# Performance work log

Measured on AMD Instinct MI355X. Metric: run time of the kernel, lower is better.

The kernel has to match this reference:

```python
import jax, jax.numpy as jnp
import numpy as np

N, E, D, MH, C, L = 50000, 800000, 256, 256, 47, 3
BN_EPS = 1e-5
NORM_EPS = 1e-12


def setup_inputs() -> dict:
    key = jax.random.key(0)
    ks = jax.random.split(key, 20)
    s = 0.05
    inp = {
        "x": jax.random.normal(ks[0], (N, D), jnp.float32),
        "edge_index": jax.random.randint(ks[1], (2, E), 0, N, jnp.int64),
        "lin_l_W": jax.random.normal(ks[2], (L, D, D), jnp.float32) * s,
        "lin_l_b": jnp.zeros((L, D), jnp.float32),
        "lin_r_W": jax.random.normal(ks[3], (L, D, D), jnp.float32) * s,
        "lin_r_b": jnp.zeros((L, D), jnp.float32),
        "mlp_W1": jax.random.normal(ks[4], (L, D, MH), jnp.float32) * s,
        "mlp_b1": jnp.zeros((L, MH), jnp.float32),
        "blk_Wa": jax.random.normal(ks[5], (L, 2, MH, MH), jnp.float32) * s,
        "blk_ba": jnp.zeros((L, 2, MH), jnp.float32),
        "blk_gamma": jnp.ones((L, 2, MH), jnp.float32),
        "blk_beta": jnp.zeros((L, 2, MH), jnp.float32),
        "blk_Wb": jax.random.normal(ks[6], (L, 2, MH, MH), jnp.float32) * s,
        "blk_bb": jnp.zeros((L, 2, MH), jnp.float32),
        "mlp_W2": jax.random.normal(ks[7], (L, MH, D), jnp.float32) * s,
        "mlp_b2": jnp.zeros((L, D), jnp.float32),
        "post_W1": jax.random.normal(ks[8], (D, D), jnp.float32) * s,
        "post_b1": jnp.zeros((D,), jnp.float32),
        "post_W2": jax.random.normal(ks[9], (D, C), jnp.float32) * s,
        "post_b2": jnp.zeros((C,), jnp.float32),
    }
    return inp


def _model(x, edge_index, lin_l_W, lin_l_b, lin_r_W, lin_r_b, mlp_W1, mlp_b1,
           blk_Wa, blk_ba, blk_gamma, blk_beta, blk_Wb, blk_bb, mlp_W2, mlp_b2,
           post_W1, post_b1, post_W2, post_b2):
    src, dst = edge_index[0], edge_index[1]
    n = x.shape[0]
    # in-degree counts for scatter-mean (torch_scatter clamps count to >=1)
    cnt = jax.ops.segment_sum(jnp.ones((src.shape[0],), x.dtype), dst, num_segments=n)
    cnt = jnp.maximum(cnt, 1.0)[:, None]
    inv_bn = 1.0 / jnp.sqrt(1.0 + BN_EPS)  # eval BN with running mean=0, var=1
    for i in range(L):
        # gather source features, scatter-mean at destinations
        z = jax.ops.segment_sum(x[src], dst, num_segments=n) / cnt  # [N, d]
        prop = x @ lin_l_W[i] + lin_l_b[i] + z @ lin_r_W[i] + lin_r_b[i]
        h = prop @ mlp_W1[i] + mlp_b1[i]
        for j in range(2):  # two ResNet blocks (dropout off at inference)
            t = h @ blk_Wa[i, j] + blk_ba[i, j]
            t = jax.nn.relu(t)
            t = blk_gamma[i, j] * (t * inv_bn) + blk_beta[i, j]
            t = t @ blk_Wb[i, j] + blk_bb[i, j]
            h = h + t
        o = h @ mlp_W2[i] + mlp_b2[i]
        # F.normalize: row-wise L2 with eps clamp
        o = o / jnp.maximum(jnp.linalg.norm(o, axis=1, keepdims=True), NORM_EPS)
        x = jax.nn.relu(o)
    h = x @ post_W1 + post_b1
    h = h @ post_W2 + post_b2
    return jax.nn.log_softmax(h, axis=1)


def reference(x, edge_index, lin_l_W, lin_l_b, lin_r_W, lin_r_b, mlp_W1, mlp_b1,
              blk_Wa, blk_ba, blk_gamma, blk_beta, blk_Wb, blk_bb, mlp_W2, mlp_b2,
              post_W1, post_b1, post_W2, post_b2):
    return _model(x, edge_index, lin_l_W, lin_l_b, lin_r_W, lin_r_b, mlp_W1, mlp_b1,
                  blk_Wa, blk_ba, blk_gamma, blk_beta, blk_Wb, blk_bb, mlp_W2, mlp_b2,
                  post_W1, post_b1, post_W2, post_b2)
```

## Files before the change

### kernel.cpp

```cpp
#include <hip/hip_runtime.h>
#include <hip/hip_bf16.h>
#include <math.h>


constexpr int DIM = 256;
constexpr int NCLS = 47;

typedef short short8 __attribute__((ext_vector_type(8)));
typedef float f32x4 __attribute__((ext_vector_type(4)));

__device__ __forceinline__ float4 ld4(const float* p) { return *(const float4*)p; }

__device__ __forceinline__ void split_bf16(float a, short& hi, short& lo) {
    unsigned u = __float_as_uint(a);
    unsigned r = (u + 0x7fffu + ((u >> 16) & 1u)) & 0xffff0000u;
    hi = (short)(r >> 16);
    float f = a - __uint_as_float(r);
    unsigned u2 = __float_as_uint(f);
    lo = (short)((u2 + 0x7fffu + ((u2 >> 16) & 1u)) >> 16);
}

__device__ __forceinline__ void split8(const float4& u0, const float4& u1,
                                       short8& hi, short8& lo) {
    union { unsigned w[4]; short8 s; } H, L;
    float va[8] = {u0.x, u0.y, u0.z, u0.w, u1.x, u1.y, u1.z, u1.w};
#pragma unroll
    for (int p = 0; p < 4; ++p) {
        float a = va[2 * p], b = va[2 * p + 1];
        __hip_bfloat162 h2 = __float22bfloat162_rn(make_float2(a, b));
        float ra = a - __bfloat162float(h2.x);
        float rb = b - __bfloat162float(h2.y);
        __hip_bfloat162 l2 = __float22bfloat162_rn(make_float2(ra, rb));
        H.w[p] = *reinterpret_cast<unsigned*>(&h2);
        L.w[p] = *reinterpret_cast<unsigned*>(&l2);
    }
    hi = H.s; lo = L.s;
}

__device__ __forceinline__ int swz(int r, int c) {
    return (r << 8) + (((((c >> 2) ^ (r & 7)) & 63) << 2) | (c & 3));
}


__global__ void hist_kernel(const int* __restrict__ ei, int* __restrict__ cnt, int E) {
    int g = blockIdx.x * blockDim.x + threadIdx.x;
    if (g < E) atomicAdd(&cnt[ei[E + g]], 1);
}

__global__ __launch_bounds__(256) void scan_part(const int* __restrict__ cnt,
                                                 int* __restrict__ bsum, int n) {
    int t = threadIdx.x;
    int i0 = blockIdx.x * 1024 + t * 4;
    int4 v = make_int4(0, 0, 0, 0);
    if (i0 + 3 < n) v = *(const int4*)&cnt[i0];
    else {
        if (i0 < n) v.x = cnt[i0];
        if (i0 + 1 < n) v.y = cnt[i0 + 1];
        if (i0 + 2 < n) v.z = cnt[i0 + 2];
        if (i0 + 3 < n) v.w = cnt[i0 + 3];
    }
    int s = v.x + v.y + v.z + v.w;
#pragma unroll
    for (int off = 1; off < 64; off <<= 1) s += __shfl_xor(s, off);
    __shared__ int ws[4];
    if ((t & 63) == 0) ws[t >> 6] = s;
    __syncthreads();
    if (t == 0) bsum[blockIdx.x] = ws[0] + ws[1] + ws[2] + ws[3];
}

__global__ void scan_bsum(int* __restrict__ bsum, int nb) {
    int lane = threadIdx.x;
    int orig = (lane < nb) ? bsum[lane] : 0;
    int incl = orig;
#pragma unroll
    for (int off = 1; off < 64; off <<= 1) {
        int u = __shfl_up(incl, off);
        if (lane >= off) incl += u;
    }
    if (lane < nb) bsum[lane] = incl - orig;
}

__global__ __launch_bounds__(256) void scan_final(const int* __restrict__ cnt,
                                                  const int* __restrict__ bsum,
                                                  int* __restrict__ rowptr,
                                                  int* __restrict__ cursor,
                                                  float* __restrict__ invc, int n, int E) {
    int t = threadIdx.x;
    int lane = t & 63, wv = t >> 6;
    int i0 = blockIdx.x * 1024 + t * 4;
    int4 v = make_int4(0, 0, 0, 0);
    if (i0 + 3 < n) v = *(const int4*)&cnt[i0];
    else {
        if (i0 < n) v.x = cnt[i0];
        if (i0 + 1 < n) v.y = cnt[i0 + 1];
        if (i0 + 2 < n) v.z = cnt[i0 + 2];
        if (i0 + 3 < n) v.w = cnt[i0 + 3];
    }
    int s = v.x + v.y + v.z + v.w;
    int incl = s;
#pragma unroll
    for (int off = 1; off < 64; off <<= 1) {
        int u = __shfl_up(incl, off);
        if (lane >= off) incl += u;
    }
    __shared__ int wtot[4];
    if (lane == 63) wtot[wv] = incl;
    __syncthreads();
    int woff = 0;
    for (int w = 0; w < 4; ++w) woff += (w < wv) ? wtot[w] : 0;
    int p = bsum[blockIdx.x] + woff + incl - s;
    int vv[4] = {v.x, v.y, v.z, v.w};
#pragma unroll
    for (int j = 0; j < 4; ++j) {
        int i = i0 + j;
        if (i < n) {
            rowptr[i] = p;
            cursor[i] = p;
            int c = vv[j];
            invc[i] = 1.0f / (float)(c > 0 ? c : 1);
            p += c;
        }
    }
    if (blockIdx.x == 0 && t == 0) rowptr[n] = E;
}

__global__ void fill_kernel(const int* __restrict__ ei, int* __restrict__ cursor,
                            int* __restrict__ colb, int E) {
    int g = blockIdx.x * blockDim.x + threadIdx.x;
    if (g < E) {
        int s = ei[g];
        int d = ei[E + g];
        int p = atomicAdd(&cursor[d], 1);
        colb[p] = s;
    }
}

__global__ __launch_bounds__(256) void gather_mean(const float* __restrict__ x,
                                                   const int* __restrict__ rowptr,
                                                   const int* __restrict__ colb,
                                                   const float* __restrict__ invc,
                                                   float* __restrict__ z, int n) {
    int gw = (blockIdx.x * 256 + threadIdx.x) >> 6;
    int lane = threadIdx.x & 63;
    int nw = (gridDim.x * 256) >> 6;
    for (int r = gw; r < n; r += nw) {
        int p0 = rowptr[r], p1 = rowptr[r + 1];
        float a0 = 0.f, a1 = 0.f, a2 = 0.f, a3 = 0.f;
        for (int p = p0; p < p1; ++p) {
            int s = colb[p];
            float4 v = ld4(&x[(size_t)s * DIM + lane * 4]);
            a0 += v.x; a1 += v.y; a2 += v.z; a3 += v.w;
        }
        float iv = invc[r];
        *(float4*)&z[(size_t)r * DIM + lane * 4] = make_float4(a0 * iv, a1 * iv, a2 * iv, a3 * iv);
    }
}

__global__ __launch_bounds__(256) void conv_w_kernel(const float* __restrict__ W,
                                                     short* __restrict__ out, int nmat) {
    int idx = blockIdx.x * 256 + threadIdx.x;
    if (idx >= nmat * 8192) return;
    int m = idx >> 13;
    int e = idx & 8191;
    int kt = e >> 10;
    int ct = (e >> 6) & 15;
    int lane = e & 63;
    int k0 = kt * 32 + ((lane >> 4) << 3);
    int col = ct * 16 + (lane & 15);
    const float* Wm = W + (size_t)m * 65536;
    short8 hi, lo;
#pragma unroll
    for (int j = 0; j < 8; ++j) {
        short h, l;
        split_bf16(Wm[(size_t)(k0 + j) * 256 + col], h, l);
        hi[j] = h; lo[j] = l;
    }
    short* hp = out + (size_t)m * 131072 + (size_t)e * 8;
    *(short8*)hp = hi;
    *(short8*)(hp + 65536) = lo;
}

__global__ __launch_bounds__(256) void conv_w2_kernel(const float* __restrict__ W,
                                                      short* __restrict__ out) {
    int e = blockIdx.x * 256 + threadIdx.x;
    if (e >= 2048) return;
    int kt = e >> 8;
    int ct = (e >> 6) & 3;
    int lane = e & 63;
    int k0 = kt * 32 + ((lane >> 4) << 3);
    int col = ct * 16 + (lane & 15);
    short8 hi, lo;
#pragma unroll
    for (int j = 0; j < 8; ++j) {
        float v = (col < NCLS) ? W[(size_t)(k0 + j) * NCLS + col] : 0.f;
        short h, l;
        split_bf16(v, h, l);
        hi[j] = h; lo[j] = l;
    }
    short* hp = out + (size_t)e * 8;
    *(short8*)hp = hi;
    *(short8*)(hp + 16384) = lo;
}


__device__ __forceinline__ void mma_global(f32x4 (&acc)[2][8], const float* __restrict__ A,
                                           const short* __restrict__ Wf,
                                           int row0, int nrows, int wm, int wn, int lane) {
    const int lr = lane & 15;
    const int lk = (lane >> 4) << 3;
#pragma unroll
    for (int kt = 0; kt < 8; ++kt) {
        short8 ahi[2], alo[2];
#pragma unroll
        for (int mi = 0; mi < 2; ++mi) {
            int r = row0 + wm * 32 + mi * 16 + lr;
            float4 u0 = make_float4(0.f, 0.f, 0.f, 0.f), u1 = u0;
            if (r < nrows) {
                const float* ap = A + (size_t)r * DIM + kt * 32 + lk;
                u0 = ld4(ap);
                u1 = ld4(ap + 4);
            }
            split8(u0, u1, ahi[mi], alo[mi]);
        }
        const short* wb = Wf + (((size_t)(kt * 16 + wn * 8) * 64 + lane) << 3);
#pragma unroll
        for (int n = 0; n < 8; ++n) {
            short8 bhi = *(const short8*)(wb + n * 512);
            short8 blo = *(const short8*)(wb + n * 512 + 65536);
#pragma unroll
            for (int mi = 0; mi < 2; ++mi) {
                acc[mi][n] = __builtin_amdgcn_mfma_f32_16x16x32_bf16(ahi[mi], bhi, acc[mi][n], 0, 0, 0);
                acc[mi][n] = __builtin_amdgcn_mfma_f32_16x16x32_bf16(ahi[mi], blo, acc[mi][n], 0, 0, 0);
                acc[mi][n] = __builtin_amdgcn_mfma_f32_16x16x32_bf16(alo[mi], bhi, acc[mi][n], 0, 0, 0);
            }
        }
    }
}

__device__ __forceinline__ void mma_lds(f32x4 (&acc)[2][8], const float* sAf,
                                        const short* __restrict__ Wf,
                                        int wm, int wn, int lane) {
    const int lr = lane & 15;
    const int lk = (lane >> 4) << 3;
#pragma unroll
    for (int kt = 0; kt < 8; ++kt) {
        short8 ahi[2], alo[2];
#pragma unroll
        for (int mi = 0; mi < 2; ++mi) {
            int r = wm * 32 + mi * 16 + lr;
            int k0 = kt * 32 + lk;
            const float* ap0 = sAf + (r << 8) + ((((k0 >> 2) ^ (r & 7)) & 63) << 2);
            const float* ap1 = sAf + (r << 8) + (((((k0 + 4) >> 2) ^ (r & 7)) & 63) << 2);
            float4 u0 = *(const float4*)ap0;
            float4 u1 = *(const float4*)ap1;
            split8(u0, u1, ahi[mi], alo[mi]);
        }
        const short* wb = Wf + (((size_t)(kt * 16 + wn * 8) * 64 + lane) << 3);
#pragma unroll
        for (int n = 0; n < 8; ++n) {
            short8 bhi = *(const short8*)(wb + n * 512);
            short8 blo = *(const short8*)(wb + n * 512 + 65536);
#pragma unroll
            for (int mi = 0; mi < 2; ++mi) {
                acc[mi][n] = __builtin_amdgcn_mfma_f32_16x16x32_bf16(ahi[mi], bhi, acc[mi][n], 0, 0, 0);
                acc[mi][n] = __builtin_amdgcn_mfma_f32_16x16x32_bf16(ahi[mi], blo, acc[mi][n], 0, 0, 0);
                acc[mi][n] = __builtin_amdgcn_mfma_f32_16x16x32_bf16(alo[mi], bhi, acc[mi][n], 0, 0, 0);
            }
        }
    }
}

__global__ __launch_bounds__(256, 2) void layer_fused(
    const float* __restrict__ xin, const float* __restrict__ zin,
    const short* __restrict__ Wll, const short* __restrict__ Wlr,
    const short* __restrict__ Wm1,
    const short* __restrict__ Wa0, const short* __restrict__ Wb0f,
    const short* __restrict__ Wa1, const short* __restrict__ Wb1f,
    const short* __restrict__ Wm2,
    const float* __restrict__ b_ll, const float* __restrict__ b_lr,
    const float* __restrict__ b_m1,
    const float* __restrict__ b_a0, const float* __restrict__ gam0,
    const float* __restrict__ bet0, const float* __restrict__ b_b0,
    const float* __restrict__ b_a1, const float* __restrict__ gam1,
    const float* __restrict__ bet1, const float* __restrict__ b_b1,
    const float* __restrict__ b_m2,
    float bnscale, float* __restrict__ xout, int nrows) {
    __shared__ float sAf[64 * 256];
    const int tid = threadIdx.x;
    const int lane = tid & 63;
    const int wv = tid >> 6;
    const int wm = wv & 1;
    const int wn = wv >> 1;
    const int row0 = blockIdx.x * 64;
    const int lr = lane & 15;
    const int rbase = (lane >> 4) << 2;

    f32x4 acc[2][8];
    float hreg[2][8][4];

    auto zeroacc = [&]() {
#pragma unroll
        for (int mi = 0; mi < 2; ++mi)
#pragma unroll
            for (int n = 0; n < 8; ++n) acc[mi][n] = (f32x4){0.f, 0.f, 0.f, 0.f};
    };
    auto store = [&](auto f) {
        __syncthreads();
#pragma unroll
        for (int mi = 0; mi < 2; ++mi)
#pragma unroll
            for (int reg = 0; reg < 4; ++reg) {
                int r = wm * 32 + mi * 16 + rbase + reg;
#pragma unroll
                for (int n = 0; n < 8; ++n)
                    sAf[swz(r, wn * 128 + n * 16 + lr)] = f(mi, n, reg);
            }
        __syncthreads();
    };

    zeroacc();
    mma_global(acc, xin, Wll, row0, nrows, wm, wn, lane);
    mma_global(acc, zin, Wlr, row0, nrows, wm, wn, lane);
    {
        float bias[8];
#pragma unroll
        for (int n = 0; n < 8; ++n) {
            int c = wn * 128 + n * 16 + lr;
            bias[n] = b_ll[c] + b_lr[c];
        }
        store([&](int mi, int n, int reg) { return acc[mi][n][reg] + bias[n]; });
    }
    zeroacc();
    mma_lds(acc, sAf, Wm1, wm, wn, lane);
    {
        float bias[8];
#pragma unroll
        for (int n = 0; n < 8; ++n) bias[n] = b_m1[wn * 128 + n * 16 + lr];
        store([&](int mi, int n, int reg) {
            float v = acc[mi][n][reg] + bias[n];
            hreg[mi][n][reg] = v;
            return v;
        });
    }
    const short* Was[2] = {Wa0, Wa1};
    const short* Wbs[2] = {Wb0f, Wb1f};
    const float* bas[2] = {b_a0, b_a1};
    const float* gms[2] = {gam0, gam1};
    const float* bes[2] = {bet0, bet1};
    const float* bbs[2] = {b_b0, b_b1};
    for (int j = 0; j < 2; ++j) {
        zeroacc();
        mma_lds(acc, sAf, Was[j], wm, wn, lane);
        {
            float ba[8], gm[8], be[8];
#pragma unroll
            for (int n = 0; n < 8; ++n) {
                int c = wn * 128 + n * 16 + lr;
                ba[n] = bas[j][c];
                gm[n] = gms[j][c] * bnscale;
                be[n] = bes[j][c];
            }
            store([&](int mi, int n, int reg) {
                return fmaf(fmaxf(acc[mi][n][reg] + ba[n], 0.f), gm[n], be[n]);
            });
        }
        zeroacc();
        mma_lds(acc, sAf, Wbs[j], wm, wn, lane);
        {
            float bb[8];
#pragma unroll
            for (int n = 0; n < 8; ++n) bb[n] = bbs[j][wn * 128 + n * 16 + lr];
            store([&](int mi, int n, int reg) {
                float v = hreg[mi][n][reg] + acc[mi][n][reg] + bb[n];
                hreg[mi][n][reg] = v;
                return v;
            });
        }
    }
    zeroacc();
    mma_lds(acc, sAf, Wm2, wm, wn, lane);
    {
        float bias[8];
#pragma unroll
        for (int n = 0; n < 8; ++n) bias[n] = b_m2[wn * 128 + n * 16 + lr];
        float sqs[2][4];
#pragma unroll
        for (int mi = 0; mi < 2; ++mi) {
            float sq[4] = {0.f, 0.f, 0.f, 0.f};
#pragma unroll
            for (int n = 0; n < 8; ++n)
#pragma unroll
                for (int reg = 0; reg < 4; ++reg) {
                    float v = acc[mi][n][reg] + bias[n];
                    acc[mi][n][reg] = v;
                    sq[reg] = fmaf(v, v, sq[reg]);
                }
#pragma unroll
            for (int reg = 0; reg < 4; ++reg) {
                float s = sq[reg];
                s += __shfl_xor(s, 1);
                s += __shfl_xor(s, 2);
                s += __shfl_xor(s, 4);
                s += __shfl_xor(s, 8);
                sqs[mi][reg] = s;
            }
        }
        __syncthreads();
        float* sn = sAf;
        if (lr == 0) {
#pragma unroll
            for (int mi = 0; mi < 2; ++mi)
#pragma unroll
                for (int reg = 0; reg < 4; ++reg)
                    sn[wn * 64 + wm * 32 + mi * 16 + rbase + reg] = sqs[mi][reg];
        }
        __syncthreads();
#pragma unroll
        for (int mi = 0; mi < 2; ++mi)
#pragma unroll
            for (int reg = 0; reg < 4; ++reg) {
                int ridx = wm * 32 + mi * 16 + rbase + reg;
                int r = row0 + ridx;
                float s = sn[ridx] + sn[64 + ridx];
                float inv = 1.0f / fmaxf(sqrtf(s), 1e-12f);
                if (r < nrows) {
#pragma unroll
                    for (int n = 0; n < 8; ++n) {
                        int col = wn * 128 + n * 16 + lr;
                        xout[(size_t)r * DIM + col] = fmaxf(acc[mi][n][reg] * inv, 0.f);
                    }
                }
            }
    }
}

__global__ __launch_bounds__(256, 2) void post_head(
    const float* __restrict__ xin, const short* __restrict__ WpF,
    const float* __restrict__ pb1, const short* __restrict__ W2f,
    const float* __restrict__ pb2, float* __restrict__ out, int nrows) {
    __shared__ float sAf[64 * 256];
    const int tid = threadIdx.x;
    const int lane = tid & 63;
    const int wv = tid >> 6;
    const int wm = wv & 1;
    const int wn = wv >> 1;
    const int row0 = blockIdx.x * 64;
    const int lr = lane & 15;
    const int lk = (lane >> 4) << 3;
    const int rbase = (lane >> 4) << 2;

    f32x4 acc[2][8];
#pragma unroll
    for (int mi = 0; mi < 2; ++mi)
#pragma unroll
        for (int n = 0; n < 8; ++n) acc[mi][n] = (f32x4){0.f, 0.f, 0.f, 0.f};
    mma_global(acc, xin, WpF, row0, nrows, wm, wn, lane);
    {
        float bias[8];
#pragma unroll
        for (int n = 0; n < 8; ++n) bias[n] = pb1[wn * 128 + n * 16 + lr];
        __syncthreads();
#pragma unroll
        for (int mi = 0; mi < 2; ++mi)
#pragma unroll
            for (int reg = 0; reg < 4; ++reg) {
                int r = wm * 32 + mi * 16 + rbase + reg;
#pragma unroll
                for (int n = 0; n < 8; ++n)
                    sAf[swz(r, wn * 128 + n * 16 + lr)] = acc[mi][n][reg] + bias[n];
            }
        __syncthreads();
    }
    f32x4 hacc[4];
#pragma unroll
    for (int n = 0; n < 4; ++n) hacc[n] = (f32x4){0.f, 0.f, 0.f, 0.f};
#pragma unroll
    for (int kt = 0; kt < 8; ++kt) {
        int r = wv * 16 + lr;
        int k0 = kt * 32 + lk;
        const float* ap0 = sAf + (r << 8) + ((((k0 >> 2) ^ (r & 7)) & 63) << 2);
        const float* ap1 = sAf + (r << 8) + (((((k0 + 4) >> 2) ^ (r & 7)) & 63) << 2);
        float4 u0 = *(const float4*)ap0;
        float4 u1 = *(const float4*)ap1;
        short8 ahi, alo;
        split8(u0, u1, ahi, alo);
        const short* wb = W2f + (((size_t)kt * 4 * 64 + lane) << 3);
#pragma unroll
        for (int n = 0; n < 4; ++n) {
            short8 bhi = *(const short8*)(wb + n * 512);
            short8 blo = *(const short8*)(wb + n * 512 + 16384);
            hacc[n] = __builtin_amdgcn_mfma_f32_16x16x32_bf16(ahi, bhi, hacc[n], 0, 0, 0);
            hacc[n] = __builtin_amdgcn_mfma_f32_16x16x32_bf16(ahi, blo, hacc[n], 0, 0, 0);
            hacc[n] = __builtin_amdgcn_mfma_f32_16x16x32_bf16(alo, bhi, hacc[n], 0, 0, 0);
        }
    }
    float bias[4];
#pragma unroll
    for (int n = 0; n < 4; ++n) {
        int col = n * 16 + lr;
        bias[n] = (col < NCLS) ? pb2[col] : 0.f;
    }
#pragma unroll
    for (int reg = 0; reg < 4; ++reg) {
        float v[4];
        float m = -INFINITY;
#pragma unroll
        for (int n = 0; n < 4; ++n) {
            int col = n * 16 + lr;
            v[n] = (col < NCLS) ? (hacc[n][reg] + bias[n]) : -INFINITY;
            m = fmaxf(m, v[n]);
        }
        m = fmaxf(m, __shfl_xor(m, 1));
        m = fmaxf(m, __shfl_xor(m, 2));
        m = fmaxf(m, __shfl_xor(m, 4));
        m = fmaxf(m, __shfl_xor(m, 8));
        float e = 0.f;
#pragma unroll
        for (int n = 0; n < 4; ++n) e += (v[n] > -INFINITY) ? expf(v[n] - m) : 0.f;
        e += __shfl_xor(e, 1);
        e += __shfl_xor(e, 2);
        e += __shfl_xor(e, 4);
        e += __shfl_xor(e, 8);
        float lse = m + logf(e);
        int r = row0 + wv * 16 + rbase + reg;
        if (r < nrows) {
#pragma unroll
            for (int n = 0; n < 4; ++n) {
                int col = n * 16 + lr;
                if (col < NCLS) out[(size_t)r * NCLS + col] = v[n] - lse;
            }
        }
    }
}


extern "C" void kernel_launch(void* const* d_in, const int* in_sizes, int n_in,
                              void* d_out, int out_size, void* d_ws, size_t ws_size,
                              hipStream_t stream) {
    const float* x_in = (const float*)d_in[0];
    const int* ei = (const int*)d_in[1];
    const float* linlW = (const float*)d_in[2];
    const float* linlb = (const float*)d_in[3];
    const float* linrW = (const float*)d_in[4];
    const float* linrb = (const float*)d_in[5];
    const float* W1 = (const float*)d_in[6];
    const float* b1 = (const float*)d_in[7];
    const float* blkWa = (const float*)d_in[8];
    const float* blkba = (const float*)d_in[9];
    const float* blkg = (const float*)d_in[10];
    const float* blkbt = (const float*)d_in[11];
    const float* blkWb = (const float*)d_in[12];
    const float* blkbb = (const float*)d_in[13];
    const float* W2 = (const float*)d_in[14];
    const float* b2 = (const float*)d_in[15];
    const float* pW1 = (const float*)d_in[16];
    const float* pb1 = (const float*)d_in[17];
    const float* pW2 = (const float*)d_in[18];
    const float* pb2 = (const float*)d_in[19];

    const int n = in_sizes[0] / DIM;
    const int E = in_sizes[1] / 2;

    char* ws = (char*)d_ws;
    size_t off = 0;
    auto take = [&](size_t bytes) {
        void* p = ws + off;
        off += (bytes + 255) & ~(size_t)255;
        return p;
    };
    float* bufA = (float*)take((size_t)n * DIM * 4);
    float* bufD = (float*)take((size_t)n * DIM * 4);
    float* bufZ = (float*)take((size_t)n * DIM * 4);
    int* cnt = (int*)take((size_t)n * 4);
    int* rowptr = (int*)take((size_t)(n + 1) * 4);
    int* cursor = (int*)take((size_t)n * 4);
    float* invc = (float*)take((size_t)n * 4);
    int* colb = (int*)take((size_t)E * 4);
    int* bsum = (int*)take(256 * 4);
    short* wbuf = (short*)take((size_t)25 * 131072 * 2);
    short* w2buf = (short*)take((size_t)32768 * 2);
    (void)ws_size; (void)n_in; (void)out_size;

    const float bnscale = 0.999995000037f;

    auto WF = [&](int m) { return wbuf + (size_t)m * 131072; };
    conv_w_kernel<<<3 * 32, 256, 0, stream>>>(linlW, WF(0), 3);
    conv_w_kernel<<<3 * 32, 256, 0, stream>>>(linrW, WF(3), 3);
    conv_w_kernel<<<3 * 32, 256, 0, stream>>>(W1, WF(6), 3);
    conv_w_kernel<<<6 * 32, 256, 0, stream>>>(blkWa, WF(9), 6);
    conv_w_kernel<<<6 * 32, 256, 0, stream>>>(blkWb, WF(15), 6);
    conv_w_kernel<<<3 * 32, 256, 0, stream>>>(W2, WF(21), 3);
    conv_w_kernel<<<1 * 32, 256, 0, stream>>>(pW1, WF(24), 1);
    conv_w2_kernel<<<8, 256, 0, stream>>>(pW2, w2buf);

    hipMemsetAsync(cnt, 0, (size_t)n * 4, stream);
    hist_kernel<<<(E + 255) / 256, 256, 0, stream>>>(ei, cnt, E);
    const int nb = (n + 1023) / 1024;
    scan_part<<<nb, 256, 0, stream>>>(cnt, bsum, n);
    scan_bsum<<<1, 64, 0, stream>>>(bsum, nb);
    scan_final<<<nb, 256, 0, stream>>>(cnt, bsum, rowptr, cursor, invc, n, E);
    fill_kernel<<<(E + 255) / 256, 256, 0, stream>>>(ei, cursor, colb, E);

    const int gblocks = (n + 63) / 64;
    const float* xcur = x_in;
    float* xbufs[2] = {bufA, bufD};
    for (int i = 0; i < 3; ++i) {
        gather_mean<<<(n + 3) / 4, 256, 0, stream>>>(xcur, rowptr, colb, invc, bufZ, n);
        int wo = i * 2;
        float* xo = xbufs[i & 1];
        layer_fused<<<gblocks, 256, 0, stream>>>(
            xcur, bufZ,
            WF(0 + i), WF(3 + i), WF(6 + i),
            WF(9 + wo), WF(15 + wo), WF(9 + wo + 1), WF(15 + wo + 1),
            WF(21 + i),
            linlb + i * 256, linrb + i * 256, b1 + i * 256,
            blkba + wo * 256, blkg + wo * 256, blkbt + wo * 256, blkbb + wo * 256,
            blkba + (wo + 1) * 256, blkg + (wo + 1) * 256, blkbt + (wo + 1) * 256,
            blkbb + (wo + 1) * 256,
            b2 + i * 256, bnscale, xo, n);
        xcur = xo;
    }
    post_head<<<gblocks, 256, 0, stream>>>(xcur, WF(24), pb1, w2buf, pb2, (float*)d_out, n);
}
```

Before: 1.577 ms.

## Enlarge fused layer tile to 128 rows with 512-thread blocks

```diff
diff --git a/kernel.cpp b/kernel.cpp
--- a/kernel.cpp
+++ b/kernel.cpp
@@ -270,7 +270,7 @@
     }
 }
 
-__global__ __launch_bounds__(256, 2) void layer_fused(
+__global__ __launch_bounds__(512, 2) void layer_fused(
     const float* __restrict__ xin, const float* __restrict__ zin,
     const short* __restrict__ Wll, const short* __restrict__ Wlr,
     const short* __restrict__ Wm1,
@@ -285,13 +285,13 @@
     const float* __restrict__ bet1, const float* __restrict__ b_b1,
     const float* __restrict__ b_m2,
     float bnscale, float* __restrict__ xout, int nrows) {
-    __shared__ float sAf[64 * 256];
+    extern __shared__ float sAf[];
     const int tid = threadIdx.x;
     const int lane = tid & 63;
     const int wv = tid >> 6;
-    const int wm = wv & 1;
-    const int wn = wv >> 1;
-    const int row0 = blockIdx.x * 64;
+    const int wm = wv & 3;
+    const int wn = wv >> 2;
+    const int row0 = blockIdx.x * 128;
     const int lr = lane & 15;
     const int rbase = (lane >> 4) << 2;
 
@@ -342,41 +342,39 @@
             return v;
         });
     }
-    const short* Was[2] = {Wa0, Wa1};
-    const short* Wbs[2] = {Wb0f, Wb1f};
-    const float* bas[2] = {b_a0, b_a1};
-    const float* gms[2] = {gam0, gam1};
-    const float* bes[2] = {bet0, bet1};
-    const float* bbs[2] = {b_b0, b_b1};
-    for (int j = 0; j < 2; ++j) {
+    auto resblk = [&](const short* Wa, const short* Wbf, const float* ba_p,
+                      const float* gm_p, const float* be_p, const float* bb_p) {
         zeroacc();
-        mma_lds(acc, sAf, Was[j], wm, wn, lane);
+        mma_lds(acc, sAf, Wa, wm, wn, lane);
         {
             float ba[8], gm[8], be[8];
 #pragma unroll
             for (int n = 0; n < 8; ++n) {
                 int c = wn * 128 + n * 16 + lr;
-                ba[n] = bas[j][c];
-                gm[n] = gms[j][c] * bnscale;
-                be[n] = bes[j][c];
+                ba[n] = ba_p[c];
+                gm[n] = gm_p[c] * bnscale;
+                be[n] = be_p[c];
             }
             store([&](int mi, int n, int reg) {
                 return fmaf(fmaxf(acc[mi][n][reg] + ba[n], 0.f), gm[n], be[n]);
             });
         }
         zeroacc();
-        mma_lds(acc, sAf, Wbs[j], wm, wn, lane);
+        mma_lds(acc, sAf, Wbf, wm, wn, lane);
         {
             float bb[8];
 #pragma unroll
-            for (int n = 0; n < 8; ++n) bb[n] = bbs[j][wn * 128 + n * 16 + lr];
+            for (int n = 0; n < 8; ++n) bb[n] = bb_p[wn * 128 + n * 16 + lr];
             store([&](int mi, int n, int reg) {
                 float v = hreg[mi][n][reg] + acc[mi][n][reg] + bb[n];
                 hreg[mi][n][reg] = v;
                 return v;
             });
         }
-    }
+    };
+    resblk(Wa0, Wb0f, b_a0, gam0, bet0, b_b0);
+    resblk(Wa1, Wb1f, b_a1, gam1, bet1, b_b1);
+
     zeroacc();
     mma_lds(acc, sAf, Wm2, wm, wn, lane);
     {
@@ -412,7 +410,7 @@
             for (int mi = 0; mi < 2; ++mi)
 #pragma unroll
                 for (int reg = 0; reg < 4; ++reg)
-                    sn[wn * 64 + wm * 32 + mi * 16 + rbase + reg] = sqs[mi][reg];
+                    sn[wn * 128 + wm * 32 + mi * 16 + rbase + reg] = sqs[mi][reg];
         }
         __syncthreads();
 #pragma unroll
@@ -421,7 +419,7 @@
             for (int reg = 0; reg < 4; ++reg) {
                 int ridx = wm * 32 + mi * 16 + rbase + reg;
                 int r = row0 + ridx;
-                float s = sn[ridx] + sn[64 + ridx];
+                float s = sn[ridx] + sn[128 + ridx];
                 float inv = 1.0f / fmaxf(sqrtf(s), 1e-12f);
                 if (r < nrows) {
 #pragma unroll
@@ -583,6 +581,9 @@
 
     const float bnscale = 0.999995000037f;
 
+    hipFuncSetAttribute((const void*)layer_fused,
+                        hipFuncAttributeMaxDynamicSharedMemorySize, 131072);
+
     auto WF = [&](int m) { return wbuf + (size_t)m * 131072; };
     conv_w_kernel<<<3 * 32, 256, 0, stream>>>(linlW, WF(0), 3);
     conv_w_kernel<<<3 * 32, 256, 0, stream>>>(linrW, WF(3), 3);
@@ -601,14 +602,15 @@
     scan_final<<<nb, 256, 0, stream>>>(cnt, bsum, rowptr, cursor, invc, n, E);
     fill_kernel<<<(E + 255) / 256, 256, 0, stream>>>(ei, cursor, colb, E);
 
-    const int gblocks = (n + 63) / 64;
+    const int gb128 = (n + 127) / 128;
+    const int gb64 = (n + 63) / 64;
     const float* xcur = x_in;
     float* xbufs[2] = {bufA, bufD};
     for (int i = 0; i < 3; ++i) {
         gather_mean<<<(n + 3) / 4, 256, 0, stream>>>(xcur, rowptr, colb, invc, bufZ, n);
         int wo = i * 2;
         float* xo = xbufs[i & 1];
-        layer_fused<<<gblocks, 256, 0, stream>>>(
+        layer_fused<<<gb128, 512, 131072, stream>>>(
             xcur, bufZ,
             WF(0 + i), WF(3 + i), WF(6 + i),
             WF(9 + wo), WF(15 + wo), WF(9 + wo + 1), WF(15 + wo + 1),
@@ -620,5 +622,5 @@
             b2 + i * 256, bnscale, xo, n);
         xcur = xo;
     }
-    post_head<<<gblocks, 256, 0, stream>>>(xcur, WF(24), pb1, w2buf, pb2, (float*)d_out, n);
-}
+    post_head<<<gb64, 256, 0, stream>>>(xcur, WF(24), pb1, w2buf, pb2, (float*)d_out, n);
+}
```

Measured after the change: 2.076 ms. +31.7%, slower.
